# Kernel optimization log

Measured on AMD Instinct MI355X. Metric: run time of the kernel, lower is better.

The kernel has to match this reference:

```python
import jax, jax.numpy as jnp
import numpy as np


def _lstm_layer(x_sbi, w_ih, w_hh, b):
    """Custom LSTM layer with elu candidate/cell activations.
    x_sbi: [S, B, I]; w_ih: [4H, I]; w_hh: [4H, H]; b: [4H]. Gate order i,f,g,o.
    Returns outputs [S, B, H].
    """
    H = w_hh.shape[1]
    S, B, _ = x_sbi.shape
    # Precompute the input projection for all timesteps at once.
    xw = jnp.einsum('sbi,gi->sbg', x_sbi, w_ih) + b  # [S, B, 4H]

    def step(carry, xt):
        h, c = carry
        gates = xt + h @ w_hh.T  # [B, 4H]
        i = jax.nn.sigmoid(gates[:, 0 * H:1 * H])
        f = jax.nn.sigmoid(gates[:, 1 * H:2 * H])
        g = jax.nn.elu(gates[:, 2 * H:3 * H])      # custom cell activation
        o = jax.nn.sigmoid(gates[:, 3 * H:4 * H])
        c = f * c + i * g
        h = o * jax.nn.elu(c)                       # custom hidden activation
        return (h, c), h

    h0 = jnp.zeros((B, H), dtype=x_sbi.dtype)
    c0 = jnp.zeros((B, H), dtype=x_sbi.dtype)
    _, out = jax.lax.scan(step, (h0, c0), xw)
    return out  # [S, B, H]


def setup_inputs() -> dict:
    key = jax.random.key(0)
    ks = jax.random.split(key, 12)
    B, S, I, H = 256, 512, 64, 512
    s_in = 1.0 / np.sqrt(H)
    d = {
        'x': jax.random.normal(ks[0], (B, S, I), dtype=jnp.float32),
        'w_ih1': jax.random.normal(ks[1], (4 * H, I), dtype=jnp.float32) * s_in,
        'w_hh1': jax.random.normal(ks[2], (4 * H, H), dtype=jnp.float32) * s_in,
        'b1': jax.random.normal(ks[3], (4 * H,), dtype=jnp.float32) * s_in,
        'w_ih2': jax.random.normal(ks[4], (4 * H, H), dtype=jnp.float32) * s_in,
        'w_hh2': jax.random.normal(ks[5], (4 * H, H), dtype=jnp.float32) * s_in,
        'b2': jax.random.normal(ks[6], (4 * H,), dtype=jnp.float32) * s_in,
        'w_ih3': jax.random.normal(ks[7], (4 * H, H), dtype=jnp.float32) * s_in,
        'w_hh3': jax.random.normal(ks[8], (4 * H, H), dtype=jnp.float32) * s_in,
        'b3': jax.random.normal(ks[9], (4 * H,), dtype=jnp.float32) * s_in,
        'fc_w': jax.random.normal(ks[10], (1, H), dtype=jnp.float32) * s_in,
        'fc_b': jax.random.normal(ks[11], (1,), dtype=jnp.float32) * s_in,
    }
    return d


def reference(x, w_ih1, w_hh1, b1, w_ih2, w_hh2, b2, w_ih3, w_hh3, b3, fc_w, fc_b):
    # x: [B, S, I] -> seq-first [S, B, I] (matches torch permute(1,0,2))
    out = jnp.transpose(x, (1, 0, 2))
    out = _lstm_layer(out, w_ih1, w_hh1, b1)  # dropout = identity (eval)
    out = _lstm_layer(out, w_ih2, w_hh2, b2)
    out = _lstm_layer(out, w_ih3, w_hh3, b3)
    last = out[-1]                             # [B, H]
    return last @ fc_w.T + fc_b                # [B, 1]
```

## Files before the change

kernel.cpp:

```cpp
#include <hip/hip_runtime.h>
#include <stdint.h>
#include <stddef.h>

#define S_LEN 512
#define BATCH 256
#define NIN   64
#define HD    512
#define G4    2048

typedef _Float16 f16;
typedef _Float16 f16x8 __attribute__((ext_vector_type(8)));
typedef float    f32x4 __attribute__((ext_vector_type(4)));
typedef uint32_t u32x4 __attribute__((ext_vector_type(4)));

__global__ void k_f32_to_f16(const float* __restrict__ src, f16* __restrict__ dst, int n) {
  int i = blockIdx.x * 256 + threadIdx.x;
  if (i < n) dst[i] = (f16)src[i];
}

__global__ void k_x_transpose(const float* __restrict__ x, f16* __restrict__ xin) {
  int idx = blockIdx.x * 256 + threadIdx.x;
  int i  = idx & 63;
  int sb = idx >> 6;
  int b  = sb & 255;
  int s  = sb >> 8;
  xin[idx] = (f16)x[((size_t)b * S_LEN + s) * NIN + i];
}

__global__ void k_zero_i32(uint32_t* p, int n) {
  int i = blockIdx.x * 256 + threadIdx.x;
  if (i < n) p[i] = 0u;
}

template<int K>
__global__ __launch_bounds__(256) void k_proj(const f16* __restrict__ A,
                                              const f16* __restrict__ W,
                                              const float* __restrict__ bias,
                                              f16* __restrict__ C) {
  constexpr int PITCH = 40;
  __shared__ f16 lA[128 * PITCH];
  __shared__ f16 lB[128 * PITCH];
  const int m0 = blockIdx.x * 128;
  const int n0 = blockIdx.y * 128;
  const int tid  = threadIdx.x;
  const int lane = tid & 63;
  const int wave = tid >> 6;
  const int wm = (wave & 1) * 64;
  const int wn = (wave >> 1) * 64;
  const int ln = lane & 15;
  const int quad = lane >> 4;
  const int r  = tid >> 1;
  const int ce = (tid & 1) * 16;

  f32x4 acc[4][4] = {};

  for (int kb = 0; kb < K; kb += 32) {
    const f16* ga = A + (size_t)(m0 + r) * K + kb + ce;
    const f16* gb = W + (size_t)(n0 + r) * K + kb + ce;
    u32x4 a0 = *(const u32x4*)ga;
    u32x4 a1 = *(const u32x4*)(ga + 8);
    u32x4 b0 = *(const u32x4*)gb;
    u32x4 b1 = *(const u32x4*)(gb + 8);
    __syncthreads();
    *(u32x4*)&lA[r * PITCH + ce]     = a0;
    *(u32x4*)&lA[r * PITCH + ce + 8] = a1;
    *(u32x4*)&lB[r * PITCH + ce]     = b0;
    *(u32x4*)&lB[r * PITCH + ce + 8] = b1;
    __syncthreads();
    f16x8 af[4], bf[4];
#pragma unroll
    for (int i = 0; i < 4; i++) {
      af[i] = *(const f16x8*)&lA[(wm + i * 16 + ln) * PITCH + quad * 8];
      bf[i] = *(const f16x8*)&lB[(wn + i * 16 + ln) * PITCH + quad * 8];
    }
#pragma unroll
    for (int mi = 0; mi < 4; mi++)
#pragma unroll
      for (int ni = 0; ni < 4; ni++)
        acc[mi][ni] = __builtin_amdgcn_mfma_f32_16x16x32_f16(af[mi], bf[ni], acc[mi][ni], 0, 0, 0);
  }

#pragma unroll
  for (int ni = 0; ni < 4; ni++) {
    const int n = n0 + wn + ni * 16 + ln;
    const float bv = bias[n];
#pragma unroll
    for (int mi = 0; mi < 4; mi++) {
#pragma unroll
      for (int rr = 0; rr < 4; rr++) {
        const int m = m0 + wm + mi * 16 + quad * 4 + rr;
        C[(size_t)m * G4 + n] = (f16)(acc[mi][ni][rr] + bv);
      }
    }
  }
}

__global__ __launch_bounds__(512, 2) void k_recur(
    const f16* __restrict__ Whh,
    const f16* __restrict__ xw,
    f16* __restrict__ ring,
    int* __restrict__ flags,
    f16* __restrict__ hclean,
    float* __restrict__ cbuf,
    int t0, int T, int cleanAll) {
  const int tid  = threadIdx.x;
  const int lane = tid & 63;
  const int wave = tid >> 6;
  const int gi = blockIdx.x >> 4;
  const int bi = blockIdx.x & 15;
  const int ln = lane & 15;
  const int quad = lane >> 4;

  __shared__ f16  lh[16 * 520];
  __shared__ float lgate[16 * 132];

  const int grow = (wave >> 1) * HD + gi * 32 + (wave & 1) * 16 + ln;
  f16x8 wf[16];
#pragma unroll
  for (int ks = 0; ks < 16; ks++) {
    u32x4 t = *(const u32x4*)(Whh + (size_t)grow * HD + ks * 32 + quad * 8);
    asm volatile("" : "+v"(t));
    wf[ks] = __builtin_bit_cast(f16x8, t);
  }

  const int b_  = tid >> 5;
  const int hl_ = tid & 31;
  float cv = 0.f;
  if (t0 != 0) cv = cbuf[(size_t)(bi * 16 + b_) * HD + gi * 32 + hl_];

  const int* fl = flags + bi * 16;
  int* myflag = flags + bi * 16 + gi;
  uint64_t* lh64 = (uint64_t*)lh;

  for (int tt = 0; tt < T; tt++) {
    const int t = t0 + tt;

    const f16* xwp = xw + (size_t)(tt * 256 + bi * 16 + b_) * G4 + gi * 32 + hl_;
    float xg0 = (float)xwp[0];
    float xg1 = (float)xwp[512];
    float xg2 = (float)xwp[1024];
    float xg3 = (float)xwp[1536];

    {
      int v = __hip_atomic_load(fl + (lane & 15), __ATOMIC_RELAXED, __HIP_MEMORY_SCOPE_AGENT);
      while (!__all(v >= t)) {
        __builtin_amdgcn_s_sleep(1);
        v = __hip_atomic_load(fl + (lane & 15), __ATOMIC_RELAXED, __HIP_MEMORY_SCOPE_AGENT);
      }
    }
    asm volatile("" ::: "memory");

    const uint64_t* hin64 = (const uint64_t*)(ring + (size_t)(t & 3) * (BATCH * HD)
                                              + (size_t)(bi * 16) * HD);
    uint64_t d[4];
#pragma unroll
    for (int j = 0; j < 4; j++)
      d[j] = __hip_atomic_load(hin64 + j * 512 + tid, __ATOMIC_RELAXED, __HIP_MEMORY_SCOPE_AGENT);
#pragma unroll
    for (int j = 0; j < 4; j++) {
      const int e   = j * 512 + tid;
      const int row = e >> 7;
      const int c8  = e & 127;
      lh64[row * 130 + c8] = d[j];
    }
    __syncthreads();

    f32x4 acc = {0.f, 0.f, 0.f, 0.f};
#pragma unroll
    for (int ks = 0; ks < 16; ks++) {
      f16x8 af = *(const f16x8*)&lh[ln * 520 + ks * 32 + quad * 8];
      acc = __builtin_amdgcn_mfma_f32_16x16x32_f16(af, wf[ks], acc, 0, 0, 0);
    }
    const int gcol = (wave >> 1) * 32 + (wave & 1) * 16 + ln;
#pragma unroll
    for (int rr = 0; rr < 4; rr++)
      lgate[(quad * 4 + rr) * 132 + gcol] = acc[rr];
    __syncthreads();

    {
      float gi_ = lgate[b_ * 132 + 0  + hl_] + xg0;
      float gf_ = lgate[b_ * 132 + 32 + hl_] + xg1;
      float gg_ = lgate[b_ * 132 + 64 + hl_] + xg2;
      float go_ = lgate[b_ * 132 + 96 + hl_] + xg3;
      const float ig = 1.f / (1.f + expf(-gi_));
      const float fg = 1.f / (1.f + expf(-gf_));
      const float gg = gg_ > 0.f ? gg_ : expm1f(gg_);
      const float og = 1.f / (1.f + expf(-go_));
      cv = fg * cv + ig * gg;
      const float hv = og * (cv > 0.f ? cv : expm1f(cv));
      f16 hv16 = (f16)hv;
      unsigned short us;
      __builtin_memcpy(&us, &hv16, 2);
      const size_t col = (size_t)(bi * 16 + b_) * HD + gi * 32 + hl_;
      __hip_atomic_store((unsigned short*)(ring + (size_t)((t + 1) & 3) * (BATCH * HD) + col),
                         us, __ATOMIC_RELAXED, __HIP_MEMORY_SCOPE_AGENT);
      if (cleanAll)
        hclean[(size_t)(tt * 256 + bi * 16 + b_) * HD + gi * 32 + hl_] = hv16;
      else if (tt == T - 1)
        hclean[(size_t)(bi * 16 + b_) * HD + gi * 32 + hl_] = hv16;
    }
    __syncthreads();
    if (tid == 0)
      __hip_atomic_store(myflag, t + 1, __ATOMIC_RELAXED, __HIP_MEMORY_SCOPE_AGENT);
  }

  cbuf[(size_t)(bi * 16 + b_) * HD + gi * 32 + hl_] = cv;
}

__global__ __launch_bounds__(64) void k_fc(const f16* __restrict__ hlast,
                                           const float* __restrict__ fcw,
                                           const float* __restrict__ fcb,
                                           float* __restrict__ out) {
  const int b = blockIdx.x, lane = threadIdx.x;
  const f16* hp = hlast + (size_t)b * HD + lane * 8;
  float s = 0.f;
#pragma unroll
  for (int j = 0; j < 8; j++) s += (float)hp[j] * fcw[lane * 8 + j];
  for (int off = 32; off; off >>= 1) s += __shfl_down(s, off);
  if (lane == 0) out[b] = s + fcb[0];
}

extern "C" void kernel_launch(void* const* d_in, const int* in_sizes, int n_in,
                              void* d_out, int out_size, void* d_ws, size_t ws_size,
                              hipStream_t stream) {
  (void)in_sizes; (void)n_in; (void)out_size;
  const float* x      = (const float*)d_in[0];
  const float* wih[3] = {(const float*)d_in[1], (const float*)d_in[4], (const float*)d_in[7]};
  const float* whh[3] = {(const float*)d_in[2], (const float*)d_in[5], (const float*)d_in[8]};
  const float* bia[3] = {(const float*)d_in[3], (const float*)d_in[6], (const float*)d_in[9]};
  const float* fcw = (const float*)d_in[10];
  const float* fcb = (const float*)d_in[11];
  float* out = (float*)d_out;

  char* ws = (char*)d_ws;
  size_t off = 0;
  auto alloc = [&](size_t bytes) -> char* {
    off = (off + 255) & ~(size_t)255;
    char* p = ws + off;
    off += bytes;
    return p;
  };

  f16* xin = (f16*)alloc((size_t)S_LEN * BATCH * NIN * 2);
  f16* wih16[3];
  wih16[0] = (f16*)alloc((size_t)G4 * NIN * 2);
  wih16[1] = (f16*)alloc((size_t)G4 * HD * 2);
  wih16[2] = (f16*)alloc((size_t)G4 * HD * 2);
  f16* whh16[3];
  for (int l = 0; l < 3; l++) whh16[l] = (f16*)alloc((size_t)G4 * HD * 2);
  float* cbuf[3];
  for (int l = 0; l < 3; l++) cbuf[l] = (float*)alloc((size_t)BATCH * HD * 4);
  f16* ring[3];
  for (int l = 0; l < 3; l++) ring[l] = (f16*)alloc((size_t)4 * BATCH * HD * 2);
  int* flags = (int*)alloc(3 * 256 * 4);
  f16* hclean2 = (f16*)alloc((size_t)BATCH * HD * 2);

  int T = 64;
  while (T > 4) {
    size_t need = off + 8 * 256
                + 2 * ((size_t)T * BATCH * HD * 2 + 256)
                + (size_t)T * BATCH * G4 * 2;
    if (need <= ws_size) break;
    T >>= 1;
  }
  f16* hclean01[2];
  hclean01[0] = (f16*)alloc((size_t)T * BATCH * HD * 2);
  hclean01[1] = (f16*)alloc((size_t)T * BATCH * HD * 2);
  f16* xw = (f16*)alloc((size_t)T * BATCH * G4 * 2);

  {
    int n = S_LEN * BATCH * NIN;
    k_x_transpose<<<dim3(n / 256), dim3(256), 0, stream>>>(x, xin);
  }
  k_f32_to_f16<<<dim3((G4 * NIN + 255) / 256), dim3(256), 0, stream>>>(wih[0], wih16[0], G4 * NIN);
  k_f32_to_f16<<<dim3((G4 * HD + 255) / 256), dim3(256), 0, stream>>>(wih[1], wih16[1], G4 * HD);
  k_f32_to_f16<<<dim3((G4 * HD + 255) / 256), dim3(256), 0, stream>>>(wih[2], wih16[2], G4 * HD);
  for (int l = 0; l < 3; l++)
    k_f32_to_f16<<<dim3((G4 * HD + 255) / 256), dim3(256), 0, stream>>>(whh[l], whh16[l], G4 * HD);
  for (int l = 0; l < 3; l++)
    k_zero_i32<<<dim3(BATCH * HD / 2 / 256), dim3(256), 0, stream>>>((uint32_t*)ring[l],
                                                                     BATCH * HD / 2);
  k_zero_i32<<<dim3(3), dim3(256), 0, stream>>>((uint32_t*)flags, 3 * 256);

  for (int t0 = 0; t0 < S_LEN; t0 += T) {
    for (int l = 0; l < 3; l++) {
      dim3 pg(T * BATCH / 128, G4 / 128);
      if (l == 0) {
        const f16* Achunk = xin + (size_t)t0 * BATCH * NIN;
        k_proj<NIN><<<pg, dim3(256), 0, stream>>>(Achunk, wih16[0], bia[0], xw);
      } else {
        k_proj<HD><<<pg, dim3(256), 0, stream>>>(hclean01[l - 1], wih16[l], bia[l], xw);
      }
      f16* hc = (l == 2) ? hclean2 : hclean01[l];
      k_recur<<<dim3(256), dim3(512), 0, stream>>>(whh16[l], xw, ring[l], flags + l * 256,
                                                   hc, cbuf[l], t0, T, l != 2);
    }
  }

  k_fc<<<dim3(BATCH), dim3(64), 0, stream>>>(hclean2, fcw, fcb, out);
}
```

Before: 5.469 ms.

## Fuse all three LSTM layers into one persistent wavefront-pipelined kernel

Replaces the chunked per-layer projection GEMM plus recurrence launches with a single persistent kernel of 768 blocks, one group of 256 per layer. Each block keeps both W_hh and W_ih slices in registers and computes the input projection on the fly from the previous layer's hidden state. Layers run as a wavefront, synchronised through per-layer flags and a 32-deep ring buffer. This removes the separate projection GEMMs, the xw and hclean traffic and many kernel launches, and lets the three layers overlap in time. In exchange it doubles the MFMA work per step, raises register pressure, and relies on all 768 blocks being co-resident, or the spin-waits could deadlock.

```diff
diff --git a/kernel.cpp b/kernel.cpp
--- a/kernel.cpp
+++ b/kernel.cpp
@@ -7,6 +7,7 @@
 #define NIN   64
 #define HD    512
 #define G4    2048
+#define RING_D 32
 
 typedef _Float16 f16;
 typedef _Float16 f16x8 __attribute__((ext_vector_type(8)));
@@ -32,136 +33,123 @@
   if (i < n) p[i] = 0u;
 }
 
-template<int K>
-__global__ __launch_bounds__(256) void k_proj(const f16* __restrict__ A,
-                                              const f16* __restrict__ W,
-                                              const float* __restrict__ bias,
-                                              f16* __restrict__ C) {
-  constexpr int PITCH = 40;
-  __shared__ f16 lA[128 * PITCH];
-  __shared__ f16 lB[128 * PITCH];
-  const int m0 = blockIdx.x * 128;
-  const int n0 = blockIdx.y * 128;
+__global__ __launch_bounds__(512, 6) void k_fused(
+    const f16* __restrict__ whh,
+    const f16* __restrict__ wih,
+    const float* __restrict__ b0,
+    const float* __restrict__ b1,
+    const float* __restrict__ b2,
+    const f16* __restrict__ xin,
+    f16* __restrict__ ring,
+    int* __restrict__ flags,
+    f16* __restrict__ hlast) {
   const int tid  = threadIdx.x;
   const int lane = tid & 63;
   const int wave = tid >> 6;
-  const int wm = (wave & 1) * 64;
-  const int wn = (wave >> 1) * 64;
-  const int ln = lane & 15;
+  const int l    = blockIdx.x >> 8;
+  const int idx  = blockIdx.x & 255;
+  const int gi   = idx >> 4;
+  const int bi   = idx & 15;
+  const int ln   = lane & 15;
   const int quad = lane >> 4;
-  const int r  = tid >> 1;
-  const int ce = (tid & 1) * 16;
-
-  f32x4 acc[4][4] = {};
-
-  for (int kb = 0; kb < K; kb += 32) {
-    const f16* ga = A + (size_t)(m0 + r) * K + kb + ce;
-    const f16* gb = W + (size_t)(n0 + r) * K + kb + ce;
-    u32x4 a0 = *(const u32x4*)ga;
-    u32x4 a1 = *(const u32x4*)(ga + 8);
-    u32x4 b0 = *(const u32x4*)gb;
-    u32x4 b1 = *(const u32x4*)(gb + 8);
-    __syncthreads();
-    *(u32x4*)&lA[r * PITCH + ce]     = a0;
-    *(u32x4*)&lA[r * PITCH + ce + 8] = a1;
-    *(u32x4*)&lB[r * PITCH + ce]     = b0;
-    *(u32x4*)&lB[r * PITCH + ce + 8] = b1;
-    __syncthreads();
-    f16x8 af[4], bf[4];
-#pragma unroll
-    for (int i = 0; i < 4; i++) {
-      af[i] = *(const f16x8*)&lA[(wm + i * 16 + ln) * PITCH + quad * 8];
-      bf[i] = *(const f16x8*)&lB[(wn + i * 16 + ln) * PITCH + quad * 8];
-    }
-#pragma unroll
-    for (int mi = 0; mi < 4; mi++)
-#pragma unroll
-      for (int ni = 0; ni < 4; ni++)
-        acc[mi][ni] = __builtin_amdgcn_mfma_f32_16x16x32_f16(af[mi], bf[ni], acc[mi][ni], 0, 0, 0);
-  }
-
-#pragma unroll
-  for (int ni = 0; ni < 4; ni++) {
-    const int n = n0 + wn + ni * 16 + ln;
-    const float bv = bias[n];
-#pragma unroll
-    for (int mi = 0; mi < 4; mi++) {
-#pragma unroll
-      for (int rr = 0; rr < 4; rr++) {
-        const int m = m0 + wm + mi * 16 + quad * 4 + rr;
-        C[(size_t)m * G4 + n] = (f16)(acc[mi][ni][rr] + bv);
-      }
-    }
-  }
-}
-
-__global__ __launch_bounds__(512, 2) void k_recur(
-    const f16* __restrict__ Whh,
-    const f16* __restrict__ xw,
-    f16* __restrict__ ring,
-    int* __restrict__ flags,
-    f16* __restrict__ hclean,
-    float* __restrict__ cbuf,
-    int t0, int T, int cleanAll) {
-  const int tid  = threadIdx.x;
-  const int lane = tid & 63;
-  const int wave = tid >> 6;
-  const int gi = blockIdx.x >> 4;
-  const int bi = blockIdx.x & 15;
-  const int ln = lane & 15;
-  const int quad = lane >> 4;
-
-  __shared__ f16  lh[16 * 520];
+
+  __shared__ f16   lh [16 * 520];
+  __shared__ f16   lhp[16 * 520];
   __shared__ float lgate[16 * 132];
 
+  const f16* whh_l = whh + (size_t)l * G4 * HD;
+  const f16* wih_l = wih + (size_t)l * G4 * HD;
+  const float* bias_l = (l == 0) ? b0 : (l == 1 ? b1 : b2);
+
   const int grow = (wave >> 1) * HD + gi * 32 + (wave & 1) * 16 + ln;
-  f16x8 wf[16];
+  f16x8 wfh[16];
 #pragma unroll
   for (int ks = 0; ks < 16; ks++) {
-    u32x4 t = *(const u32x4*)(Whh + (size_t)grow * HD + ks * 32 + quad * 8);
+    u32x4 t = *(const u32x4*)(whh_l + (size_t)grow * HD + ks * 32 + quad * 8);
     asm volatile("" : "+v"(t));
-    wf[ks] = __builtin_bit_cast(f16x8, t);
+    wfh[ks] = __builtin_bit_cast(f16x8, t);
+  }
+  f16x8 wfi[16];
+  if (l == 0) {
+#pragma unroll
+    for (int ks = 0; ks < 2; ks++) {
+      u32x4 t = *(const u32x4*)(wih_l + (size_t)grow * NIN + ks * 32 + quad * 8);
+      asm volatile("" : "+v"(t));
+      wfi[ks] = __builtin_bit_cast(f16x8, t);
+    }
+  } else {
+#pragma unroll
+    for (int ks = 0; ks < 16; ks++) {
+      u32x4 t = *(const u32x4*)(wih_l + (size_t)grow * HD + ks * 32 + quad * 8);
+      asm volatile("" : "+v"(t));
+      wfi[ks] = __builtin_bit_cast(f16x8, t);
+    }
   }
 
   const int b_  = tid >> 5;
   const int hl_ = tid & 31;
   float cv = 0.f;
-  if (t0 != 0) cv = cbuf[(size_t)(bi * 16 + b_) * HD + gi * 32 + hl_];
-
-  const int* fl = flags + bi * 16;
-  int* myflag = flags + bi * 16 + gi;
-  uint64_t* lh64 = (uint64_t*)lh;
-
-  for (int tt = 0; tt < T; tt++) {
-    const int t = t0 + tt;
-
-    const f16* xwp = xw + (size_t)(tt * 256 + bi * 16 + b_) * G4 + gi * 32 + hl_;
-    float xg0 = (float)xwp[0];
-    float xg1 = (float)xwp[512];
-    float xg2 = (float)xwp[1024];
-    float xg3 = (float)xwp[1536];
-
-    {
-      int v = __hip_atomic_load(fl + (lane & 15), __ATOMIC_RELAXED, __HIP_MEMORY_SCOPE_AGENT);
-      while (!__all(v >= t)) {
+  const float bv0 = bias_l[0 * HD + gi * 32 + hl_];
+  const float bv1 = bias_l[1 * HD + gi * 32 + hl_];
+  const float bv2 = bias_l[2 * HD + gi * 32 + hl_];
+  const float bv3 = bias_l[3 * HD + gi * 32 + hl_];
+
+  int* fown = flags + l * 256 + bi * 16;
+  int* myflag = fown + gi;
+  const int* fprev = (l > 0) ? (flags + (l - 1) * 256 + bi * 16) : fown;
+  const int* fnext = (l < 2) ? (flags + (l + 1) * 256 + bi * 16) : fown;
+
+  uint64_t* lh64  = (uint64_t*)lh;
+  uint64_t* lhp64 = (uint64_t*)lhp;
+
+  for (int t = 0; t < S_LEN; t++) {
+    uint64_t xv = 0;
+    if (l == 0 && tid < 256) {
+      const int xr = tid >> 4, xc = tid & 15;
+      xv = *(const uint64_t*)(xin + ((size_t)(t * 256 + bi * 16 + xr)) * NIN + xc * 4);
+    }
+
+    if (wave == 0) {
+      const int* fp = fown;
+      int need = t;
+      if (quad == 1 && l > 0)      { fp = fprev; need = t + 1; }
+      else if (quad == 2 && l < 2) { fp = fnext; need = t + 2 - RING_D; }
+      int v = __hip_atomic_load(fp + ln, __ATOMIC_RELAXED, __HIP_MEMORY_SCOPE_AGENT);
+      while (!__all(v >= need)) {
         __builtin_amdgcn_s_sleep(1);
-        v = __hip_atomic_load(fl + (lane & 15), __ATOMIC_RELAXED, __HIP_MEMORY_SCOPE_AGENT);
-      }
-    }
-    asm volatile("" ::: "memory");
-
-    const uint64_t* hin64 = (const uint64_t*)(ring + (size_t)(t & 3) * (BATCH * HD)
-                                              + (size_t)(bi * 16) * HD);
-    uint64_t d[4];
+        v = __hip_atomic_load(fp + ln, __ATOMIC_RELAXED, __HIP_MEMORY_SCOPE_AGENT);
+      }
+    }
+    __syncthreads();
+
+    const uint64_t* hown = (const uint64_t*)(ring
+        + ((size_t)l * RING_D + (t & (RING_D - 1))) * (BATCH * HD)
+        + (size_t)(bi * 16) * HD);
+    uint64_t dA[4];
 #pragma unroll
     for (int j = 0; j < 4; j++)
-      d[j] = __hip_atomic_load(hin64 + j * 512 + tid, __ATOMIC_RELAXED, __HIP_MEMORY_SCOPE_AGENT);
+      dA[j] = __hip_atomic_load(hown + j * 512 + tid, __ATOMIC_RELAXED, __HIP_MEMORY_SCOPE_AGENT);
+
+    if (l > 0) {
+      const uint64_t* hprev = (const uint64_t*)(ring
+          + ((size_t)(l - 1) * RING_D + ((t + 1) & (RING_D - 1))) * (BATCH * HD)
+          + (size_t)(bi * 16) * HD);
+      uint64_t dB[4];
+#pragma unroll
+      for (int j = 0; j < 4; j++)
+        dB[j] = __hip_atomic_load(hprev + j * 512 + tid, __ATOMIC_RELAXED, __HIP_MEMORY_SCOPE_AGENT);
+#pragma unroll
+      for (int j = 0; j < 4; j++) {
+        const int e = j * 512 + tid, row = e >> 7, c8 = e & 127;
+        lhp64[row * 130 + c8] = dB[j];
+      }
+    } else {
+      if (tid < 256) lhp64[(tid >> 4) * 130 + (tid & 15)] = xv;
+    }
 #pragma unroll
     for (int j = 0; j < 4; j++) {
-      const int e   = j * 512 + tid;
-      const int row = e >> 7;
-      const int c8  = e & 127;
-      lh64[row * 130 + c8] = d[j];
+      const int e = j * 512 + tid, row = e >> 7, c8 = e & 127;
+      lh64[row * 130 + c8] = dA[j];
     }
     __syncthreads();
 
@@ -169,7 +157,20 @@
 #pragma unroll
     for (int ks = 0; ks < 16; ks++) {
       f16x8 af = *(const f16x8*)&lh[ln * 520 + ks * 32 + quad * 8];
-      acc = __builtin_amdgcn_mfma_f32_16x16x32_f16(af, wf[ks], acc, 0, 0, 0);
+      acc = __builtin_amdgcn_mfma_f32_16x16x32_f16(af, wfh[ks], acc, 0, 0, 0);
+    }
+    if (l == 0) {
+#pragma unroll
+      for (int ks = 0; ks < 2; ks++) {
+        f16x8 ap = *(const f16x8*)&lhp[ln * 520 + ks * 32 + quad * 8];
+        acc = __builtin_amdgcn_mfma_f32_16x16x32_f16(ap, wfi[ks], acc, 0, 0, 0);
+      }
+    } else {
+#pragma unroll
+      for (int ks = 0; ks < 16; ks++) {
+        f16x8 ap = *(const f16x8*)&lhp[ln * 520 + ks * 32 + quad * 8];
+        acc = __builtin_amdgcn_mfma_f32_16x16x32_f16(ap, wfi[ks], acc, 0, 0, 0);
+      }
     }
     const int gcol = (wave >> 1) * 32 + (wave & 1) * 16 + ln;
 #pragma unroll
@@ -178,33 +179,30 @@
     __syncthreads();
 
     {
-      float gi_ = lgate[b_ * 132 + 0  + hl_] + xg0;
-      float gf_ = lgate[b_ * 132 + 32 + hl_] + xg1;
-      float gg_ = lgate[b_ * 132 + 64 + hl_] + xg2;
-      float go_ = lgate[b_ * 132 + 96 + hl_] + xg3;
-      const float ig = 1.f / (1.f + expf(-gi_));
-      const float fg = 1.f / (1.f + expf(-gf_));
-      const float gg = gg_ > 0.f ? gg_ : expm1f(gg_);
-      const float og = 1.f / (1.f + expf(-go_));
-      cv = fg * cv + ig * gg;
-      const float hv = og * (cv > 0.f ? cv : expm1f(cv));
+      float gi_ = lgate[b_ * 132 + 0  + hl_] + bv0;
+      float gf_ = lgate[b_ * 132 + 32 + hl_] + bv1;
+      float gg_ = lgate[b_ * 132 + 64 + hl_] + bv2;
+      float go_ = lgate[b_ * 132 + 96 + hl_] + bv3;
+      const float igt = 1.f / (1.f + expf(-gi_));
+      const float fgt = 1.f / (1.f + expf(-gf_));
+      const float ggt = gg_ > 0.f ? gg_ : expm1f(gg_);
+      const float ogt = 1.f / (1.f + expf(-go_));
+      cv = fgt * cv + igt * ggt;
+      const float hv = ogt * (cv > 0.f ? cv : expm1f(cv));
       f16 hv16 = (f16)hv;
       unsigned short us;
       __builtin_memcpy(&us, &hv16, 2);
       const size_t col = (size_t)(bi * 16 + b_) * HD + gi * 32 + hl_;
-      __hip_atomic_store((unsigned short*)(ring + (size_t)((t + 1) & 3) * (BATCH * HD) + col),
-                         us, __ATOMIC_RELAXED, __HIP_MEMORY_SCOPE_AGENT);
-      if (cleanAll)
-        hclean[(size_t)(tt * 256 + bi * 16 + b_) * HD + gi * 32 + hl_] = hv16;
-      else if (tt == T - 1)
-        hclean[(size_t)(bi * 16 + b_) * HD + gi * 32 + hl_] = hv16;
+      __hip_atomic_store((unsigned short*)(ring
+            + ((size_t)l * RING_D + ((t + 1) & (RING_D - 1))) * (BATCH * HD) + col),
+          us, __ATOMIC_RELAXED, __HIP_MEMORY_SCOPE_AGENT);
+      if (l == 2 && t == S_LEN - 1)
+        hlast[col] = hv16;
     }
     __syncthreads();
     if (tid == 0)
       __hip_atomic_store(myflag, t + 1, __ATOMIC_RELAXED, __HIP_MEMORY_SCOPE_AGENT);
   }
-
-  cbuf[(size_t)(bi * 16 + b_) * HD + gi * 32 + hl_] = cv;
 }
 
 __global__ __launch_bounds__(64) void k_fc(const f16* __restrict__ hlast,
@@ -223,7 +221,7 @@
 extern "C" void kernel_launch(void* const* d_in, const int* in_sizes, int n_in,
                               void* d_out, int out_size, void* d_ws, size_t ws_size,
                               hipStream_t stream) {
-  (void)in_sizes; (void)n_in; (void)out_size;
+  (void)in_sizes; (void)n_in; (void)out_size; (void)ws_size;
   const float* x      = (const float*)d_in[0];
   const float* wih[3] = {(const float*)d_in[1], (const float*)d_in[4], (const float*)d_in[7]};
   const float* whh[3] = {(const float*)d_in[2], (const float*)d_in[5], (const float*)d_in[8]};
@@ -241,61 +239,29 @@
     return p;
   };
 
-  f16* xin = (f16*)alloc((size_t)S_LEN * BATCH * NIN * 2);
-  f16* wih16[3];
-  wih16[0] = (f16*)alloc((size_t)G4 * NIN * 2);
-  wih16[1] = (f16*)alloc((size_t)G4 * HD * 2);
-  wih16[2] = (f16*)alloc((size_t)G4 * HD * 2);
-  f16* whh16[3];
-  for (int l = 0; l < 3; l++) whh16[l] = (f16*)alloc((size_t)G4 * HD * 2);
-  float* cbuf[3];
-  for (int l = 0; l < 3; l++) cbuf[l] = (float*)alloc((size_t)BATCH * HD * 4);
-  f16* ring[3];
-  for (int l = 0; l < 3; l++) ring[l] = (f16*)alloc((size_t)4 * BATCH * HD * 2);
+  f16* xin   = (f16*)alloc((size_t)S_LEN * BATCH * NIN * 2);
+  f16* wih16 = (f16*)alloc((size_t)3 * G4 * HD * 2);
+  f16* whh16 = (f16*)alloc((size_t)3 * G4 * HD * 2);
+  f16* ring  = (f16*)alloc((size_t)3 * RING_D * BATCH * HD * 2);
   int* flags = (int*)alloc(3 * 256 * 4);
-  f16* hclean2 = (f16*)alloc((size_t)BATCH * HD * 2);
-
-  int T = 64;
-  while (T > 4) {
-    size_t need = off + 8 * 256
-                + 2 * ((size_t)T * BATCH * HD * 2 + 256)
-                + (size_t)T * BATCH * G4 * 2;
-    if (need <= ws_size) break;
-    T >>= 1;
-  }
-  f16* hclean01[2];
-  hclean01[0] = (f16*)alloc((size_t)T * BATCH * HD * 2);
-  hclean01[1] = (f16*)alloc((size_t)T * BATCH * HD * 2);
-  f16* xw = (f16*)alloc((size_t)T * BATCH * G4 * 2);
+  f16* hlast = (f16*)alloc((size_t)BATCH * HD * 2);
 
   {
     int n = S_LEN * BATCH * NIN;
     k_x_transpose<<<dim3(n / 256), dim3(256), 0, stream>>>(x, xin);
   }
-  k_f32_to_f16<<<dim3((G4 * NIN + 255) / 256), dim3(256), 0, stream>>>(wih[0], wih16[0], G4 * NIN);
-  k_f32_to_f16<<<dim3((G4 * HD + 255) / 256), dim3(256), 0, stream>>>(wih[1], wih16[1], G4 * HD);
-  k_f32_to_f16<<<dim3((G4 * HD + 255) / 256), dim3(256), 0, stream>>>(wih[2], wih16[2], G4 * HD);
+  k_f32_to_f16<<<dim3((G4 * NIN + 255) / 256), dim3(256), 0, stream>>>(wih[0], wih16, G4 * NIN);
+  k_f32_to_f16<<<dim3((G4 * HD + 255) / 256), dim3(256), 0, stream>>>(wih[1], wih16 + (size_t)G4 * HD, G4 * HD);
+  k_f32_to_f16<<<dim3((G4 * HD + 255) / 256), dim3(256), 0, stream>>>(wih[2], wih16 + (size_t)2 * G4 * HD, G4 * HD);
   for (int l = 0; l < 3; l++)
-    k_f32_to_f16<<<dim3((G4 * HD + 255) / 256), dim3(256), 0, stream>>>(whh[l], whh16[l], G4 * HD);
+    k_f32_to_f16<<<dim3((G4 * HD + 255) / 256), dim3(256), 0, stream>>>(whh[l], whh16 + (size_t)l * G4 * HD, G4 * HD);
   for (int l = 0; l < 3; l++)
-    k_zero_i32<<<dim3(BATCH * HD / 2 / 256), dim3(256), 0, stream>>>((uint32_t*)ring[l],
-                                                                     BATCH * HD / 2);
+    k_zero_i32<<<dim3(BATCH * HD / 2 / 256), dim3(256), 0, stream>>>(
+        (uint32_t*)(ring + (size_t)l * RING_D * BATCH * HD), BATCH * HD / 2);
   k_zero_i32<<<dim3(3), dim3(256), 0, stream>>>((uint32_t*)flags, 3 * 256);
 
-  for (int t0 = 0; t0 < S_LEN; t0 += T) {
-    for (int l = 0; l < 3; l++) {
-      dim3 pg(T * BATCH / 128, G4 / 128);
-      if (l == 0) {
-        const f16* Achunk = xin + (size_t)t0 * BATCH * NIN;
-        k_proj<NIN><<<pg, dim3(256), 0, stream>>>(Achunk, wih16[0], bia[0], xw);
-      } else {
-        k_proj<HD><<<pg, dim3(256), 0, stream>>>(hclean01[l - 1], wih16[l], bia[l], xw);
-      }
-      f16* hc = (l == 2) ? hclean2 : hclean01[l];
-      k_recur<<<dim3(256), dim3(512), 0, stream>>>(whh16[l], xw, ring[l], flags + l * 256,
-                                                   hc, cbuf[l], t0, T, l != 2);
-    }
-  }
-
-  k_fc<<<dim3(BATCH), dim3(64), 0, stream>>>(hclean2, fcw, fcb, out);
-}
+  k_fused<<<dim3(768), dim3(512), 0, stream>>>(whh16, wih16, bia[0], bia[1], bia[2],
+                                               xin, ring, flags, hlast);
+
+  k_fc<<<dim3(BATCH), dim3(64), 0, stream>>>(hlast, fcw, fcb, out);
+}
```

Measured after the change: 10.93 ms. 2x slower.
